# Kernel optimization log

Hardware: AMD Instinct MI355X
Metric: run time of the kernel (lower is better)

Reference implementation:

```python
import jax, jax.numpy as jnp
import numpy as np

N_MODES = 256
N_LAYERS = 4


def _fourier_layer(inp, x, fw_l, lw_l):
    # inp: [B, n_modes] layer state; x: [B, 3] coords
    # tf.signal.rfftnd(..., fft_length=[n_modes]) crops/pads the last axis to
    # n_modes, i.e. uses the first n_modes entries of concat([x, inp], -1).
    d = jnp.concatenate([x, inp], axis=-1)[:, :N_MODES]        # [B, n_modes]
    F = jnp.fft.rfft(d, n=N_MODES, axis=-1)                    # [B, n_modes//2+1]
    x_spatial = jnp.fft.irfft(F * fw_l.astype(F.dtype), n=N_MODES, axis=-1)
    x_spatial = x_spatial.astype(jnp.float32)
    z = inp[:, :N_MODES] * lw_l                                # linear residual branch
    return jax.nn.relu(x_spatial + z)


def setup_inputs() -> dict:
    key = jax.random.key(0)
    ks = jax.random.split(key, 6)
    B, P1, P2, P3 = 262144, 64, N_MODES, 1
    mu = jax.random.normal(ks[0], (B, P1), dtype=jnp.float32)
    x = jax.random.normal(ks[1], (B, 3), dtype=jnp.float32)
    W1 = jax.random.normal(ks[2], (P1, P2), dtype=jnp.float32) * (2.0 / P1) ** 0.5
    b1 = jnp.zeros((P2,), dtype=jnp.float32)
    fw = jax.random.normal(ks[3], (N_LAYERS, N_MODES // 2 + 1), dtype=jnp.float32)
    lw = jax.random.normal(ks[4], (N_LAYERS, N_MODES), dtype=jnp.float32) * 0.1
    W2 = jax.random.normal(ks[5], (P2, P3), dtype=jnp.float32) * (1.0 / P2) ** 0.5
    b2 = jnp.zeros((P3,), dtype=jnp.float32)
    return {"mu": mu, "x": x, "W1": W1, "b1": b1, "fw": fw, "lw": lw, "W2": W2, "b2": b2}


def reference(mu, x, W1, b1, fw, lw, W2, b2):
    # encoder (first_network): dense + relu  -> [B, p_2]
    h = jax.nn.relu(mu @ W1 + b1)
    # stack of Fourier layers (small, structurally distinct loop over n_layers)
    for l in range(N_LAYERS):
        h = _fourier_layer(h, x, fw[l], lw[l])
    # decoder (last_network): dense -> [B, p_3]
    return h @ W2 + b2
```

## Files before the change

### kernel.cpp

```cpp
#include <hip/hip_runtime.h>

#define N_B   262144
#define BM    128
#define KAUG  288
#define LDA   264

typedef _Float16 f16x8 __attribute__((ext_vector_type(8)));
typedef _Float16 f16x4 __attribute__((ext_vector_type(4)));
typedef float    f32x4 __attribute__((ext_vector_type(4)));
typedef float    f32x16 __attribute__((ext_vector_type(16)));

__global__ void fno_precompute(const float* __restrict__ W1,
                               const float* __restrict__ fw,
                               const float* __restrict__ lw,
                               _Float16* __restrict__ Mt,
                               _Float16* __restrict__ W1t)
{
    const int t = threadIdx.x;
    const int b = blockIdx.x;
    if (b < 64) {
        const int l  = b >> 4;
        const int ng = b & 15;
        __shared__ float cosTab[256];
        __shared__ float cs[256];
        cosTab[t] = cosf((float)t * (6.28318530717958647692f / 256.0f));
        __syncthreads();
        {
            const float* fwl = fw + l * 129;
            float s = fwl[0];
            #pragma unroll 4
            for (int k = 1; k < 128; ++k)
                s += 2.0f * fwl[k] * cosTab[(k * t) & 255];
            s += fwl[128] * ((t & 1) ? -1.0f : 1.0f);
            cs[t] = s * (1.0f / 256.0f);
        }
        __syncthreads();
        for (int idx = t; idx < 16 * KAUG; idx += 256) {
            const int n = ng * 16 + idx / KAUG;
            const int k = idx % KAUG;
            float v = 0.0f;
            if (k < 253)               v = cs[(n - k - 3) & 255];
            if (k == n)                v += lw[l * 256 + n];
            if (k >= 256 && k < 259)   v = cs[(n - (k - 256)) & 255];
            Mt[((size_t)l * 256 + n) * KAUG + k] = (_Float16)v;
        }
    } else {
        const int base = (b - 64) * 4096;
        #pragma unroll
        for (int i = 0; i < 16; ++i) {
            const int idx = base + t + i * 256;
            const int n = idx >> 6, k = idx & 63;
            W1t[idx] = (_Float16)W1[k * 256 + n];
        }
    }
}

__global__ __launch_bounds__(256, 2)
void fno_main(const float* __restrict__ mu,
              const float* __restrict__ x,
              const float* __restrict__ b1,
              const float* __restrict__ W2,
              const float* __restrict__ b2,
              const _Float16* __restrict__ Mt,
              const _Float16* __restrict__ W1t,
              float* __restrict__ out)
{
    __shared__ __align__(16) _Float16 hA[(BM + 1) * LDA];
    __shared__ float b1s[256];
    __shared__ float W2s[256];
    __shared__ float red[BM];

    const int t    = threadIdx.x;
    const int w    = t >> 6;
    const int lane = t & 63;
    const int i32  = lane & 31;
    const int q2   = lane >> 5;
    const int r0   = blockIdx.x * BM;
    const int hoff = i32 * LDA + 8 * q2;

    {
        const float4* mu4 = (const float4*)mu + (size_t)r0 * 16;
        #pragma unroll
        for (int j = 0; j < 8; ++j) {
            int f = t + 256 * j;
            int row = f >> 4, c4 = f & 15;
            float4 v = mu4[f];
            f16x4 h;
            h[0] = (_Float16)v.x; h[1] = (_Float16)v.y;
            h[2] = (_Float16)v.z; h[3] = (_Float16)v.w;
            *(f16x4*)&hA[row * LDA + c4 * 4] = h;
        }
        if (t < BM) {
            const float* xp = x + (size_t)(r0 + t) * 3;
            f16x8 hx = {(_Float16)xp[0], (_Float16)xp[1], (_Float16)xp[2],
                        (_Float16)0, (_Float16)0, (_Float16)0,
                        (_Float16)0, (_Float16)0};
            *(f16x8*)&hA[t * LDA + 256] = hx;
        }
        if (t < 33) {
            f16x8 z8 = {};
            *(f16x8*)&hA[BM * LDA + 8 * t] = z8;
        }
        b1s[t] = b1[t];
        W2s[t] = W2[t];
    }
    __syncthreads();

    const f32x16 fz = {0.f,0.f,0.f,0.f, 0.f,0.f,0.f,0.f,
                       0.f,0.f,0.f,0.f, 0.f,0.f,0.f,0.f};
    f32x16 acc[2][4];

    #pragma unroll
    for (int ft = 0; ft < 2; ++ft)
        #pragma unroll
        for (int rt = 0; rt < 4; ++rt) acc[ft][rt] = fz;

    {
        const _Float16* W1p = W1t + (64 * w + i32) * 64 + 8 * q2;
        #pragma unroll
        for (int kc = 0; kc < 4; ++kc) {
            f16x8 mfrag[2];
            #pragma unroll
            for (int ft = 0; ft < 2; ++ft)
                mfrag[ft] = *(const f16x8*)(W1p + 32 * ft * 64 + 16 * kc);
            #pragma unroll
            for (int rt = 0; rt < 4; ++rt) {
                f16x8 hfrag = *(const f16x8*)&hA[hoff + 32 * rt * LDA + 16 * kc];
                #pragma unroll
                for (int ft = 0; ft < 2; ++ft)
                    acc[ft][rt] = __builtin_amdgcn_mfma_f32_32x32x16_f16(
                        mfrag[ft], hfrag, acc[ft][rt], 0, 0, 0);
            }
        }
    }
    __syncthreads();
    #pragma unroll
    for (int ft = 0; ft < 2; ++ft)
        #pragma unroll
        for (int rt = 0; rt < 4; ++rt) {
            const int row = 32 * rt + i32;
            #pragma unroll
            for (int rg = 0; rg < 4; ++rg) {
                const int fb = 64 * w + 32 * ft + 4 * q2 + 8 * rg;
                const float4 bias = *(const float4*)&b1s[fb];
                f16x4 hv;
                hv[0] = (_Float16)fmaxf(acc[ft][rt][4 * rg + 0] + bias.x, 0.f);
                hv[1] = (_Float16)fmaxf(acc[ft][rt][4 * rg + 1] + bias.y, 0.f);
                hv[2] = (_Float16)fmaxf(acc[ft][rt][4 * rg + 2] + bias.z, 0.f);
                hv[3] = (_Float16)fmaxf(acc[ft][rt][4 * rg + 3] + bias.w, 0.f);
                *(f16x4*)&hA[row * LDA + fb] = hv;
            }
        }

    #pragma unroll 1
    for (int l = 0; l < 4; ++l) {
        __syncthreads();
        #pragma unroll
        for (int ft = 0; ft < 2; ++ft)
            #pragma unroll
            for (int rt = 0; rt < 4; ++rt) acc[ft][rt] = fz;

        const _Float16* Mlp = Mt + (size_t)l * 256 * KAUG
                                 + (64 * w + i32) * KAUG + 8 * q2;
        #pragma unroll
        for (int kc = 0; kc < 18; ++kc) {
            f16x8 mfrag[2];
            #pragma unroll
            for (int ft = 0; ft < 2; ++ft)
                mfrag[ft] = *(const f16x8*)(Mlp + 32 * ft * KAUG + 16 * kc);
            #pragma unroll
            for (int rt = 0; rt < 4; ++rt) {
                f16x8 hfrag = *(const f16x8*)&hA[hoff + 32 * rt * LDA + 16 * kc];
                #pragma unroll
                for (int ft = 0; ft < 2; ++ft)
                    acc[ft][rt] = __builtin_amdgcn_mfma_f32_32x32x16_f16(
                        mfrag[ft], hfrag, acc[ft][rt], 0, 0, 0);
            }
        }

        __syncthreads();
        #pragma unroll
        for (int ft = 0; ft < 2; ++ft)
            #pragma unroll
            for (int rt = 0; rt < 4; ++rt) {
                const int row = 32 * rt + i32;
                #pragma unroll
                for (int rg = 0; rg < 4; ++rg) {
                    const int fb = 64 * w + 32 * ft + 4 * q2 + 8 * rg;
                    f16x4 hv;
                    hv[0] = (_Float16)fmaxf(acc[ft][rt][4 * rg + 0], 0.f);
                    hv[1] = (_Float16)fmaxf(acc[ft][rt][4 * rg + 1], 0.f);
                    hv[2] = (_Float16)fmaxf(acc[ft][rt][4 * rg + 2], 0.f);
                    hv[3] = (_Float16)fmaxf(acc[ft][rt][4 * rg + 3], 0.f);
                    *(f16x4*)&hA[row * LDA + fb] = hv;
                }
            }
    }

    __syncthreads();
    {
        const int r  = t & 127;
        const int hf = t >> 7;
        const int n0 = hf * 128;
        float s = 0.f;
        #pragma unroll
        for (int j = 0; j < 16; ++j) {
            f16x8 v = *(const f16x8*)&hA[r * LDA + n0 + 8 * j];
            const float* wp = &W2s[n0 + 8 * j];
            s += (float)v[0] * wp[0] + (float)v[1] * wp[1]
               + (float)v[2] * wp[2] + (float)v[3] * wp[3]
               + (float)v[4] * wp[4] + (float)v[5] * wp[5]
               + (float)v[6] * wp[6] + (float)v[7] * wp[7];
        }
        if (hf) red[r] = s;
        __syncthreads();
        if (!hf) out[r0 + r] = s + red[r] + b2[0];
    }
}

extern "C" void kernel_launch(void* const* d_in, const int* in_sizes, int n_in,
                              void* d_out, int out_size, void* d_ws, size_t ws_size,
                              hipStream_t stream) {
    const float* mu = (const float*)d_in[0];
    const float* x  = (const float*)d_in[1];
    const float* W1 = (const float*)d_in[2];
    const float* b1 = (const float*)d_in[3];
    const float* fw = (const float*)d_in[4];
    const float* lw = (const float*)d_in[5];
    const float* W2 = (const float*)d_in[6];
    const float* b2 = (const float*)d_in[7];
    float* out = (float*)d_out;

    _Float16* Mt  = (_Float16*)d_ws;
    _Float16* W1t = Mt + 4 * 256 * KAUG;

    fno_precompute<<<68, 256, 0, stream>>>(W1, fw, lw, Mt, W1t);
    fno_main<<<N_B / BM, 256, 0, stream>>>(mu, x, b1, W2, b2, Mt, W1t, out);
}
```

Baseline: 248.9 us.

## Shrink row tile to 96 and software-pipeline weight fragment loads across MFMA steps

Reduces the per-block row tile from 128 to 96 (2731 blocks with clamped tail rows), shrinking accumulators and LDS so more waves can be resident and the grid spreads across more CUs. The K-loop is manually unrolled with a triple-buffered rotation of weight fragments, loading fragment k+3 while issuing MFMAs for k, and prefetching the next layer's first fragments before the barrier, to hide global-load latency. Smaller tiles mean each weight fragment is reused across fewer rows, and a tail block does partly wasted work.

```diff
diff --git a/kernel.cpp b/kernel.cpp
--- a/kernel.cpp
+++ b/kernel.cpp
@@ -1,7 +1,8 @@
 #include <hip/hip_runtime.h>
 
 #define N_B   262144
-#define BM    128
+#define BM    96
+#define NBLK  2731
 #define KAUG  288
 #define LDA   264
 
@@ -55,6 +56,25 @@
     }
 }
 
+
+#define KSTEP(M0, M1, KB)                                                   \
+    { _Pragma("unroll")                                                     \
+      for (int rt = 0; rt < 3; ++rt) {                                      \
+          f16x8 hfrag = *(const f16x8*)&hA[hoff + 32 * rt * LDA + (KB)];    \
+          acc[0][rt] = __builtin_amdgcn_mfma_f32_32x32x16_f16(              \
+              M0, hfrag, acc[0][rt], 0, 0, 0);                              \
+          acc[1][rt] = __builtin_amdgcn_mfma_f32_32x32x16_f16(              \
+              M1, hfrag, acc[1][rt], 0, 0, 0);                              \
+      } }
+
+#define LDM(M0, M1, PTR, KB)                                                \
+    { M0 = *(const f16x8*)((PTR) + (KB));                                   \
+      M1 = *(const f16x8*)((PTR) + 32 * KAUG + (KB)); }
+
+#define LDMW(M0, M1, KB)                                                    \
+    { M0 = *(const f16x8*)(W1p + (KB));                                     \
+      M1 = *(const f16x8*)(W1p + 32 * 64 + (KB)); }
+
 __global__ __launch_bounds__(256, 2)
 void fno_main(const float* __restrict__ mu,
               const float* __restrict__ x,
@@ -65,7 +85,7 @@
               const _Float16* __restrict__ W1t,
               float* __restrict__ out)
 {
-    __shared__ __align__(16) _Float16 hA[(BM + 1) * LDA];
+    __shared__ __align__(16) _Float16 hA[BM * LDA + 24];
     __shared__ float b1s[256];
     __shared__ float W2s[256];
     __shared__ float red[BM];
@@ -79,65 +99,66 @@
     const int hoff = i32 * LDA + 8 * q2;
 
     {
-        const float4* mu4 = (const float4*)mu + (size_t)r0 * 16;
-        #pragma unroll
-        for (int j = 0; j < 8; ++j) {
+        const float4* mu4 = (const float4*)mu;
+        #pragma unroll
+        for (int j = 0; j < 6; ++j) {
             int f = t + 256 * j;
             int row = f >> 4, c4 = f & 15;
-            float4 v = mu4[f];
+            int g = r0 + row; if (g > N_B - 1) g = N_B - 1;
+            float4 v = mu4[(size_t)g * 16 + c4];
             f16x4 h;
             h[0] = (_Float16)v.x; h[1] = (_Float16)v.y;
             h[2] = (_Float16)v.z; h[3] = (_Float16)v.w;
             *(f16x4*)&hA[row * LDA + c4 * 4] = h;
         }
         if (t < BM) {
-            const float* xp = x + (size_t)(r0 + t) * 3;
+            int g = r0 + t; if (g > N_B - 1) g = N_B - 1;
+            const float* xp = x + (size_t)g * 3;
             f16x8 hx = {(_Float16)xp[0], (_Float16)xp[1], (_Float16)xp[2],
                         (_Float16)0, (_Float16)0, (_Float16)0,
                         (_Float16)0, (_Float16)0};
             *(f16x8*)&hA[t * LDA + 256] = hx;
         }
-        if (t < 33) {
+        if (t < 3) {
             f16x8 z8 = {};
             *(f16x8*)&hA[BM * LDA + 8 * t] = z8;
         }
         b1s[t] = b1[t];
         W2s[t] = W2[t];
     }
+
+    const _Float16* W1p = W1t + (64 * w + i32) * 64 + 8 * q2;
+    f16x8 mA0, mA1, mB0, mB1, mC0, mC1;
+    LDMW(mA0, mA1, 0)
+    LDMW(mB0, mB1, 16)
+    LDMW(mC0, mC1, 32)
     __syncthreads();
 
     const f32x16 fz = {0.f,0.f,0.f,0.f, 0.f,0.f,0.f,0.f,
                        0.f,0.f,0.f,0.f, 0.f,0.f,0.f,0.f};
-    f32x16 acc[2][4];
+    f32x16 acc[2][3];
 
     #pragma unroll
     for (int ft = 0; ft < 2; ++ft)
         #pragma unroll
-        for (int rt = 0; rt < 4; ++rt) acc[ft][rt] = fz;
+        for (int rt = 0; rt < 3; ++rt) acc[ft][rt] = fz;
+
+    KSTEP(mA0, mA1, 0)   LDMW(mA0, mA1, 48)
+    KSTEP(mB0, mB1, 16)
+    KSTEP(mC0, mC1, 32)
+    KSTEP(mA0, mA1, 48)
 
     {
-        const _Float16* W1p = W1t + (64 * w + i32) * 64 + 8 * q2;
-        #pragma unroll
-        for (int kc = 0; kc < 4; ++kc) {
-            f16x8 mfrag[2];
-            #pragma unroll
-            for (int ft = 0; ft < 2; ++ft)
-                mfrag[ft] = *(const f16x8*)(W1p + 32 * ft * 64 + 16 * kc);
-            #pragma unroll
-            for (int rt = 0; rt < 4; ++rt) {
-                f16x8 hfrag = *(const f16x8*)&hA[hoff + 32 * rt * LDA + 16 * kc];
-                #pragma unroll
-                for (int ft = 0; ft < 2; ++ft)
-                    acc[ft][rt] = __builtin_amdgcn_mfma_f32_32x32x16_f16(
-                        mfrag[ft], hfrag, acc[ft][rt], 0, 0, 0);
-            }
-        }
+        const _Float16* M0p = Mt + (size_t)(64 * w + i32) * KAUG + 8 * q2;
+        LDM(mA0, mA1, M0p, 0)
+        LDM(mB0, mB1, M0p, 16)
+        LDM(mC0, mC1, M0p, 32)
     }
     __syncthreads();
     #pragma unroll
     for (int ft = 0; ft < 2; ++ft)
         #pragma unroll
-        for (int rt = 0; rt < 4; ++rt) {
+        for (int rt = 0; rt < 3; ++rt) {
             const int row = 32 * rt + i32;
             #pragma unroll
             for (int rg = 0; rg < 4; ++rg) {
@@ -158,31 +179,40 @@
         #pragma unroll
         for (int ft = 0; ft < 2; ++ft)
             #pragma unroll
-            for (int rt = 0; rt < 4; ++rt) acc[ft][rt] = fz;
-
-        const _Float16* Mlp = Mt + (size_t)l * 256 * KAUG
-                                 + (64 * w + i32) * KAUG + 8 * q2;
-        #pragma unroll
-        for (int kc = 0; kc < 18; ++kc) {
-            f16x8 mfrag[2];
-            #pragma unroll
-            for (int ft = 0; ft < 2; ++ft)
-                mfrag[ft] = *(const f16x8*)(Mlp + 32 * ft * KAUG + 16 * kc);
-            #pragma unroll
-            for (int rt = 0; rt < 4; ++rt) {
-                f16x8 hfrag = *(const f16x8*)&hA[hoff + 32 * rt * LDA + 16 * kc];
-                #pragma unroll
-                for (int ft = 0; ft < 2; ++ft)
-                    acc[ft][rt] = __builtin_amdgcn_mfma_f32_32x32x16_f16(
-                        mfrag[ft], hfrag, acc[ft][rt], 0, 0, 0);
-            }
+            for (int rt = 0; rt < 3; ++rt) acc[ft][rt] = fz;
+
+        const _Float16* Mlp = Mt + ((size_t)l * 256 + 64 * w + i32) * KAUG + 8 * q2;
+
+        KSTEP(mA0, mA1,   0)  LDM(mA0, mA1, Mlp,  48)
+        KSTEP(mB0, mB1,  16)  LDM(mB0, mB1, Mlp,  64)
+        KSTEP(mC0, mC1,  32)  LDM(mC0, mC1, Mlp,  80)
+        KSTEP(mA0, mA1,  48)  LDM(mA0, mA1, Mlp,  96)
+        KSTEP(mB0, mB1,  64)  LDM(mB0, mB1, Mlp, 112)
+        KSTEP(mC0, mC1,  80)  LDM(mC0, mC1, Mlp, 128)
+        KSTEP(mA0, mA1,  96)  LDM(mA0, mA1, Mlp, 144)
+        KSTEP(mB0, mB1, 112)  LDM(mB0, mB1, Mlp, 160)
+        KSTEP(mC0, mC1, 128)  LDM(mC0, mC1, Mlp, 176)
+        KSTEP(mA0, mA1, 144)  LDM(mA0, mA1, Mlp, 192)
+        KSTEP(mB0, mB1, 160)  LDM(mB0, mB1, Mlp, 208)
+        KSTEP(mC0, mC1, 176)  LDM(mC0, mC1, Mlp, 224)
+        KSTEP(mA0, mA1, 192)  LDM(mA0, mA1, Mlp, 240)
+        KSTEP(mB0, mB1, 208)  LDM(mB0, mB1, Mlp, 256)
+        KSTEP(mC0, mC1, 224)
+        KSTEP(mA0, mA1, 240)
+        KSTEP(mB0, mB1, 256)
+
+        if (l < 3) {
+            const _Float16* Mn = Mlp + 256 * KAUG;
+            LDM(mA0, mA1, Mn, 0)
+            LDM(mB0, mB1, Mn, 16)
+            LDM(mC0, mC1, Mn, 32)
         }
 
         __syncthreads();
         #pragma unroll
         for (int ft = 0; ft < 2; ++ft)
             #pragma unroll
-            for (int rt = 0; rt < 4; ++rt) {
+            for (int rt = 0; rt < 3; ++rt) {
                 const int row = 32 * rt + i32;
                 #pragma unroll
                 for (int rg = 0; rg < 4; ++rg) {
@@ -199,22 +229,25 @@
 
     __syncthreads();
     {
-        const int r  = t & 127;
-        const int hf = t >> 7;
-        const int n0 = hf * 128;
+        const int r    = t >> 1;
+        const int half = t & 1;
         float s = 0.f;
-        #pragma unroll
-        for (int j = 0; j < 16; ++j) {
-            f16x8 v = *(const f16x8*)&hA[r * LDA + n0 + 8 * j];
-            const float* wp = &W2s[n0 + 8 * j];
-            s += (float)v[0] * wp[0] + (float)v[1] * wp[1]
-               + (float)v[2] * wp[2] + (float)v[3] * wp[3]
-               + (float)v[4] * wp[4] + (float)v[5] * wp[5]
-               + (float)v[6] * wp[6] + (float)v[7] * wp[7];
-        }
-        if (hf) red[r] = s;
-        __syncthreads();
-        if (!hf) out[r0 + r] = s + red[r] + b2[0];
+        if (t < 2 * BM) {
+            const int n0 = half * 128;
+            #pragma unroll
+            for (int j = 0; j < 16; ++j) {
+                f16x8 v = *(const f16x8*)&hA[r * LDA + n0 + 8 * j];
+                const float* wp = &W2s[n0 + 8 * j];
+                s += (float)v[0] * wp[0] + (float)v[1] * wp[1]
+                   + (float)v[2] * wp[2] + (float)v[3] * wp[3]
+                   + (float)v[4] * wp[4] + (float)v[5] * wp[5]
+                   + (float)v[6] * wp[6] + (float)v[7] * wp[7];
+            }
+            if (half) red[r] = s;
+        }
+        __syncthreads();
+        if (t < 2 * BM && !half && r0 + r < N_B)
+            out[r0 + r] = s + red[r] + b2[0];
     }
 }
 
@@ -235,5 +268,5 @@
     _Float16* W1t = Mt + 4 * 256 * KAUG;
 
     fno_precompute<<<68, 256, 0, stream>>>(W1, fw, lw, Mt, W1t);
-    fno_main<<<N_B / BM, 256, 0, stream>>>(mu, x, b1, W2, b2, Mt, W1t, out);
+    fno_main<<<NBLK, 256, 0, stream>>>(mu, x, b1, W2, b2, Mt, W1t, out);
 }
```

Measured after the change: 281.5 us. 1.13x slower.

## Shrink Fourier-layer GEMM K to 256 and XOR-swizzle the LDS activation tile

Applied to the files above, without the earlier changes.

The augmented K dimension drops from 288 to 256. The three x-coordinate columns are packed into slots 253-255 of each row, and the three displaced h entries (253..255) are stashed in a side slot. Their lw residual and W2 decoder terms are then added back with scalar FMAs. This cuts MFMA work per layer by about an eighth. It also replaces the padded LDS layout with an XOR swizzle, aiming to avoid bank conflicts on fragment loads. In exchange it adds branchy special-case stores and extra fixup code.

```diff
diff --git a/kernel.cpp b/kernel.cpp
--- a/kernel.cpp
+++ b/kernel.cpp
@@ -2,8 +2,9 @@
 
 #define N_B   262144
 #define BM    128
-#define KAUG  288
+#define KD    256
 #define LDA   264
+#define LDAB  528
 
 typedef _Float16 f16x8 __attribute__((ext_vector_type(8)));
 typedef _Float16 f16x4 __attribute__((ext_vector_type(4)));
@@ -35,14 +36,17 @@
             cs[t] = s * (1.0f / 256.0f);
         }
         __syncthreads();
-        for (int idx = t; idx < 16 * KAUG; idx += 256) {
-            const int n = ng * 16 + idx / KAUG;
-            const int k = idx % KAUG;
-            float v = 0.0f;
-            if (k < 253)               v = cs[(n - k - 3) & 255];
-            if (k == n)                v += lw[l * 256 + n];
-            if (k >= 256 && k < 259)   v = cs[(n - (k - 256)) & 255];
-            Mt[((size_t)l * 256 + n) * KAUG + k] = (_Float16)v;
+        for (int idx = t; idx < 16 * KD; idx += 256) {
+            const int n = ng * 16 + (idx >> 8);
+            const int k = idx & 255;
+            float v;
+            if (k < 253) {
+                v = cs[(n - k - 3) & 255];
+                if (k == n) v += lw[l * 256 + n];
+            } else {
+                v = cs[(n - (k - 253)) & 255];
+            }
+            Mt[((size_t)l * 256 + n) * KD + k] = (_Float16)v;
         }
     } else {
         const int base = (b - 64) * 4096;
@@ -59,15 +63,16 @@
 void fno_main(const float* __restrict__ mu,
               const float* __restrict__ x,
               const float* __restrict__ b1,
+              const float* __restrict__ lw,
               const float* __restrict__ W2,
               const float* __restrict__ b2,
               const _Float16* __restrict__ Mt,
               const _Float16* __restrict__ W1t,
               float* __restrict__ out)
 {
-    __shared__ __align__(16) _Float16 hA[(BM + 1) * LDA];
+    __shared__ __align__(16) char hAb[BM * LDAB];
     __shared__ float b1s[256];
-    __shared__ float W2s[256];
+    __shared__ float W2s[260];
     __shared__ float red[BM];
 
     const int t    = threadIdx.x;
@@ -76,7 +81,7 @@
     const int i32  = lane & 31;
     const int q2   = lane >> 5;
     const int r0   = blockIdx.x * BM;
-    const int hoff = i32 * LDA + 8 * q2;
+    const int xrB  = ((i32 >> 3) & 3) << 4;
 
     {
         const float4* mu4 = (const float4*)mu + (size_t)r0 * 16;
@@ -84,25 +89,24 @@
         for (int j = 0; j < 8; ++j) {
             int f = t + 256 * j;
             int row = f >> 4, c4 = f & 15;
+            int xr = ((row >> 3) & 3) << 4;
             float4 v = mu4[f];
             f16x4 h;
             h[0] = (_Float16)v.x; h[1] = (_Float16)v.y;
             h[2] = (_Float16)v.z; h[3] = (_Float16)v.w;
-            *(f16x4*)&hA[row * LDA + c4 * 4] = h;
+            *(f16x4*)(hAb + row * LDAB + ((c4 * 8) ^ xr)) = h;
         }
         if (t < BM) {
-            const float* xp = x + (size_t)(r0 + t) * 3;
-            f16x8 hx = {(_Float16)xp[0], (_Float16)xp[1], (_Float16)xp[2],
-                        (_Float16)0, (_Float16)0, (_Float16)0,
-                        (_Float16)0, (_Float16)0};
-            *(f16x8*)&hA[t * LDA + 256] = hx;
-        }
-        if (t < 33) {
-            f16x8 z8 = {};
-            *(f16x8*)&hA[BM * LDA + 8 * t] = z8;
+            const int row = t;
+            const int xr = ((row >> 3) & 3) << 4;
+            const float* xp = x + (size_t)(r0 + row) * 3;
+            *(_Float16*)(hAb + row * LDAB + (506 ^ xr)) = (_Float16)xp[0];
+            *(_Float16*)(hAb + row * LDAB + (508 ^ xr)) = (_Float16)xp[1];
+            *(_Float16*)(hAb + row * LDAB + (510 ^ xr)) = (_Float16)xp[2];
         }
         b1s[t] = b1[t];
-        W2s[t] = W2[t];
+        W2s[t] = (t < 252) ? W2[t] : 0.0f;
+        if (t < 4) W2s[256 + t] = W2[252 + t];
     }
     __syncthreads();
 
@@ -119,17 +123,14 @@
         const _Float16* W1p = W1t + (64 * w + i32) * 64 + 8 * q2;
         #pragma unroll
         for (int kc = 0; kc < 4; ++kc) {
-            f16x8 mfrag[2];
-            #pragma unroll
-            for (int ft = 0; ft < 2; ++ft)
-                mfrag[ft] = *(const f16x8*)(W1p + 32 * ft * 64 + 16 * kc);
-            #pragma unroll
-            for (int rt = 0; rt < 4; ++rt) {
-                f16x8 hfrag = *(const f16x8*)&hA[hoff + 32 * rt * LDA + 16 * kc];
-                #pragma unroll
-                for (int ft = 0; ft < 2; ++ft)
-                    acc[ft][rt] = __builtin_amdgcn_mfma_f32_32x32x16_f16(
-                        mfrag[ft], hfrag, acc[ft][rt], 0, 0, 0);
+            f16x8 m0 = *(const f16x8*)(W1p + 16 * kc);
+            f16x8 m1 = *(const f16x8*)(W1p + 32 * 64 + 16 * kc);
+            #pragma unroll
+            for (int rt = 0; rt < 4; ++rt) {
+                f16x8 hfrag = *(const f16x8*)(hAb + (32 * rt + i32) * LDAB
+                                              + ((32 * kc + 16 * q2) ^ xrB));
+                acc[0][rt] = __builtin_amdgcn_mfma_f32_32x32x16_f16(m0, hfrag, acc[0][rt], 0, 0, 0);
+                acc[1][rt] = __builtin_amdgcn_mfma_f32_32x32x16_f16(m1, hfrag, acc[1][rt], 0, 0, 0);
             }
         }
     }
@@ -148,7 +149,12 @@
                 hv[1] = (_Float16)fmaxf(acc[ft][rt][4 * rg + 1] + bias.y, 0.f);
                 hv[2] = (_Float16)fmaxf(acc[ft][rt][4 * rg + 2] + bias.z, 0.f);
                 hv[3] = (_Float16)fmaxf(acc[ft][rt][4 * rg + 3] + bias.w, 0.f);
-                *(f16x4*)&hA[row * LDA + fb] = hv;
+                if (fb == 252) {
+                    *(_Float16*)(hAb + row * LDAB + (504 ^ xrB)) = hv[0];
+                    *(f16x4*)(hAb + row * LDAB + 512) = hv;
+                } else {
+                    *(f16x4*)(hAb + row * LDAB + ((fb * 2) ^ xrB)) = hv;
+                }
             }
         }
 
@@ -160,21 +166,29 @@
             #pragma unroll
             for (int rt = 0; rt < 4; ++rt) acc[ft][rt] = fz;
 
-        const _Float16* Mlp = Mt + (size_t)l * 256 * KAUG
-                                 + (64 * w + i32) * KAUG + 8 * q2;
-        #pragma unroll
-        for (int kc = 0; kc < 18; ++kc) {
-            f16x8 mfrag[2];
-            #pragma unroll
-            for (int ft = 0; ft < 2; ++ft)
-                mfrag[ft] = *(const f16x8*)(Mlp + 32 * ft * KAUG + 16 * kc);
-            #pragma unroll
-            for (int rt = 0; rt < 4; ++rt) {
-                f16x8 hfrag = *(const f16x8*)&hA[hoff + 32 * rt * LDA + 16 * kc];
-                #pragma unroll
-                for (int ft = 0; ft < 2; ++ft)
-                    acc[ft][rt] = __builtin_amdgcn_mfma_f32_32x32x16_f16(
-                        mfrag[ft], hfrag, acc[ft][rt], 0, 0, 0);
+        const _Float16* Mlp = Mt + ((size_t)(l * 256 + 64 * w + i32)) * KD + 8 * q2;
+        #pragma unroll
+        for (int kc = 0; kc < 16; ++kc) {
+            f16x8 m0 = *(const f16x8*)(Mlp + 16 * kc);
+            f16x8 m1 = *(const f16x8*)(Mlp + 32 * KD + 16 * kc);
+            #pragma unroll
+            for (int rt = 0; rt < 4; ++rt) {
+                f16x8 hfrag = *(const f16x8*)(hAb + (32 * rt + i32) * LDAB
+                                              + ((32 * kc + 16 * q2) ^ xrB));
+                acc[0][rt] = __builtin_amdgcn_mfma_f32_32x32x16_f16(m0, hfrag, acc[0][rt], 0, 0, 0);
+                acc[1][rt] = __builtin_amdgcn_mfma_f32_32x32x16_f16(m1, hfrag, acc[1][rt], 0, 0, 0);
+            }
+        }
+
+        if (w == 3 && q2 == 1) {
+            const float* lwp = lw + l * 256 + 253;
+            const float lw0 = lwp[0], lw1 = lwp[1], lw2 = lwp[2];
+            #pragma unroll
+            for (int rt = 0; rt < 4; ++rt) {
+                f16x4 hp = *(const f16x4*)(hAb + (32 * rt + i32) * LDAB + 512);
+                acc[1][rt][13] += lw0 * (float)hp[1];
+                acc[1][rt][14] += lw1 * (float)hp[2];
+                acc[1][rt][15] += lw2 * (float)hp[3];
             }
         }
 
@@ -192,7 +206,12 @@
                     hv[1] = (_Float16)fmaxf(acc[ft][rt][4 * rg + 1], 0.f);
                     hv[2] = (_Float16)fmaxf(acc[ft][rt][4 * rg + 2], 0.f);
                     hv[3] = (_Float16)fmaxf(acc[ft][rt][4 * rg + 3], 0.f);
-                    *(f16x4*)&hA[row * LDA + fb] = hv;
+                    if (fb == 252) {
+                        *(_Float16*)(hAb + row * LDAB + (504 ^ xrB)) = hv[0];
+                        *(f16x4*)(hAb + row * LDAB + 512) = hv;
+                    } else {
+                        *(f16x4*)(hAb + row * LDAB + ((fb * 2) ^ xrB)) = hv;
+                    }
                 }
             }
     }
@@ -202,17 +221,23 @@
         const int r  = t & 127;
         const int hf = t >> 7;
         const int n0 = hf * 128;
+        const int xr = ((r >> 3) & 3) << 4;
         float s = 0.f;
         #pragma unroll
         for (int j = 0; j < 16; ++j) {
-            f16x8 v = *(const f16x8*)&hA[r * LDA + n0 + 8 * j];
+            f16x8 v = *(const f16x8*)(hAb + r * LDAB + (((n0 + 8 * j) * 2) ^ xr));
             const float* wp = &W2s[n0 + 8 * j];
             s += (float)v[0] * wp[0] + (float)v[1] * wp[1]
                + (float)v[2] * wp[2] + (float)v[3] * wp[3]
                + (float)v[4] * wp[4] + (float)v[5] * wp[5]
                + (float)v[6] * wp[6] + (float)v[7] * wp[7];
         }
-        if (hf) red[r] = s;
+        if (hf) {
+            f16x4 st = *(const f16x4*)(hAb + r * LDAB + 512);
+            s += (float)st[0] * W2s[256] + (float)st[1] * W2s[257]
+               + (float)st[2] * W2s[258] + (float)st[3] * W2s[259];
+            red[r] = s;
+        }
         __syncthreads();
         if (!hf) out[r0 + r] = s + red[r] + b2[0];
     }
@@ -232,8 +257,8 @@
     float* out = (float*)d_out;
 
     _Float16* Mt  = (_Float16*)d_ws;
-    _Float16* W1t = Mt + 4 * 256 * KAUG;
+    _Float16* W1t = Mt + 4 * 256 * KD;
 
     fno_precompute<<<68, 256, 0, stream>>>(W1, fw, lw, Mt, W1t);
-    fno_main<<<N_B / BM, 256, 0, stream>>>(mu, x, b1, W2, b2, Mt, W1t, out);
+    fno_main<<<N_B / BM, 256, 0, stream>>>(mu, x, b1, lw, W2, b2, Mt, W1t, out);
 }
```

New measurement: 259.5 us. +4.3%, slower.

## Split row tiles across 8 waves and skip zero-padded K chunk

Applied to the files above, without the earlier changes.

Doubles the block to 512 threads, so each wave computes a 64-row by 64-feature tile instead of 128 rows. This halves the accumulator registers per wave and is meant to raise occupancy and latency hiding. The Fourier-layer K loop drops its last 16-wide chunk, which only held zero padding. The final W2 reduction is split four ways across the threads. The cost is that weight fragments are loaded twice per block from global or L2, and there are more waves taking part in each barrier.

```diff
diff --git a/kernel.cpp b/kernel.cpp
--- a/kernel.cpp
+++ b/kernel.cpp
@@ -55,7 +55,7 @@
     }
 }
 
-__global__ __launch_bounds__(256, 2)
+__global__ __launch_bounds__(512, 4)
 void fno_main(const float* __restrict__ mu,
               const float* __restrict__ x,
               const float* __restrict__ b1,
@@ -68,21 +68,23 @@
     __shared__ __align__(16) _Float16 hA[(BM + 1) * LDA];
     __shared__ float b1s[256];
     __shared__ float W2s[256];
-    __shared__ float red[BM];
+    __shared__ float red3[3][BM];
 
     const int t    = threadIdx.x;
     const int w    = t >> 6;
+    const int wf   = w & 3;
+    const int wr   = w >> 2;
     const int lane = t & 63;
     const int i32  = lane & 31;
     const int q2   = lane >> 5;
     const int r0   = blockIdx.x * BM;
-    const int hoff = i32 * LDA + 8 * q2;
+    const int hoff = (64 * wr + i32) * LDA + 8 * q2;
 
     {
         const float4* mu4 = (const float4*)mu + (size_t)r0 * 16;
         #pragma unroll
-        for (int j = 0; j < 8; ++j) {
-            int f = t + 256 * j;
+        for (int j = 0; j < 4; ++j) {
+            int f = t + 512 * j;
             int row = f >> 4, c4 = f & 15;
             float4 v = mu4[f];
             f16x4 h;
@@ -101,35 +103,30 @@
             f16x8 z8 = {};
             *(f16x8*)&hA[BM * LDA + 8 * t] = z8;
         }
-        b1s[t] = b1[t];
-        W2s[t] = W2[t];
+        if (t < 256) { b1s[t] = b1[t]; W2s[t] = W2[t]; }
     }
     __syncthreads();
 
     const f32x16 fz = {0.f,0.f,0.f,0.f, 0.f,0.f,0.f,0.f,
                        0.f,0.f,0.f,0.f, 0.f,0.f,0.f,0.f};
-    f32x16 acc[2][4];
+    f32x16 acc[2][2];
 
     #pragma unroll
     for (int ft = 0; ft < 2; ++ft)
         #pragma unroll
-        for (int rt = 0; rt < 4; ++rt) acc[ft][rt] = fz;
+        for (int rt = 0; rt < 2; ++rt) acc[ft][rt] = fz;
 
     {
-        const _Float16* W1p = W1t + (64 * w + i32) * 64 + 8 * q2;
+        const _Float16* W1p = W1t + (64 * wf + i32) * 64 + 8 * q2;
         #pragma unroll
         for (int kc = 0; kc < 4; ++kc) {
-            f16x8 mfrag[2];
-            #pragma unroll
-            for (int ft = 0; ft < 2; ++ft)
-                mfrag[ft] = *(const f16x8*)(W1p + 32 * ft * 64 + 16 * kc);
-            #pragma unroll
-            for (int rt = 0; rt < 4; ++rt) {
+            f16x8 m0 = *(const f16x8*)(W1p + 16 * kc);
+            f16x8 m1 = *(const f16x8*)(W1p + 32 * 64 + 16 * kc);
+            #pragma unroll
+            for (int rt = 0; rt < 2; ++rt) {
                 f16x8 hfrag = *(const f16x8*)&hA[hoff + 32 * rt * LDA + 16 * kc];
-                #pragma unroll
-                for (int ft = 0; ft < 2; ++ft)
-                    acc[ft][rt] = __builtin_amdgcn_mfma_f32_32x32x16_f16(
-                        mfrag[ft], hfrag, acc[ft][rt], 0, 0, 0);
+                acc[0][rt] = __builtin_amdgcn_mfma_f32_32x32x16_f16(m0, hfrag, acc[0][rt], 0, 0, 0);
+                acc[1][rt] = __builtin_amdgcn_mfma_f32_32x32x16_f16(m1, hfrag, acc[1][rt], 0, 0, 0);
             }
         }
     }
@@ -137,11 +134,11 @@
     #pragma unroll
     for (int ft = 0; ft < 2; ++ft)
         #pragma unroll
-        for (int rt = 0; rt < 4; ++rt) {
-            const int row = 32 * rt + i32;
+        for (int rt = 0; rt < 2; ++rt) {
+            const int row = 64 * wr + 32 * rt + i32;
             #pragma unroll
             for (int rg = 0; rg < 4; ++rg) {
-                const int fb = 64 * w + 32 * ft + 4 * q2 + 8 * rg;
+                const int fb = 64 * wf + 32 * ft + 4 * q2 + 8 * rg;
                 const float4 bias = *(const float4*)&b1s[fb];
                 f16x4 hv;
                 hv[0] = (_Float16)fmaxf(acc[ft][rt][4 * rg + 0] + bias.x, 0.f);
@@ -158,23 +155,18 @@
         #pragma unroll
         for (int ft = 0; ft < 2; ++ft)
             #pragma unroll
-            for (int rt = 0; rt < 4; ++rt) acc[ft][rt] = fz;
-
-        const _Float16* Mlp = Mt + (size_t)l * 256 * KAUG
-                                 + (64 * w + i32) * KAUG + 8 * q2;
-        #pragma unroll
-        for (int kc = 0; kc < 18; ++kc) {
-            f16x8 mfrag[2];
-            #pragma unroll
-            for (int ft = 0; ft < 2; ++ft)
-                mfrag[ft] = *(const f16x8*)(Mlp + 32 * ft * KAUG + 16 * kc);
-            #pragma unroll
-            for (int rt = 0; rt < 4; ++rt) {
+            for (int rt = 0; rt < 2; ++rt) acc[ft][rt] = fz;
+
+        const _Float16* Mlp = Mt + ((size_t)l * 256 + 64 * wf + i32) * KAUG + 8 * q2;
+        #pragma unroll
+        for (int kc = 0; kc < 17; ++kc) {
+            f16x8 m0 = *(const f16x8*)(Mlp + 16 * kc);
+            f16x8 m1 = *(const f16x8*)(Mlp + 32 * KAUG + 16 * kc);
+            #pragma unroll
+            for (int rt = 0; rt < 2; ++rt) {
                 f16x8 hfrag = *(const f16x8*)&hA[hoff + 32 * rt * LDA + 16 * kc];
-                #pragma unroll
-                for (int ft = 0; ft < 2; ++ft)
-                    acc[ft][rt] = __builtin_amdgcn_mfma_f32_32x32x16_f16(
-                        mfrag[ft], hfrag, acc[ft][rt], 0, 0, 0);
+                acc[0][rt] = __builtin_amdgcn_mfma_f32_32x32x16_f16(m0, hfrag, acc[0][rt], 0, 0, 0);
+                acc[1][rt] = __builtin_amdgcn_mfma_f32_32x32x16_f16(m1, hfrag, acc[1][rt], 0, 0, 0);
             }
         }
 
@@ -182,11 +174,11 @@
         #pragma unroll
         for (int ft = 0; ft < 2; ++ft)
             #pragma unroll
-            for (int rt = 0; rt < 4; ++rt) {
-                const int row = 32 * rt + i32;
+            for (int rt = 0; rt < 2; ++rt) {
+                const int row = 64 * wr + 32 * rt + i32;
                 #pragma unroll
                 for (int rg = 0; rg < 4; ++rg) {
-                    const int fb = 64 * w + 32 * ft + 4 * q2 + 8 * rg;
+                    const int fb = 64 * wf + 32 * ft + 4 * q2 + 8 * rg;
                     f16x4 hv;
                     hv[0] = (_Float16)fmaxf(acc[ft][rt][4 * rg + 0], 0.f);
                     hv[1] = (_Float16)fmaxf(acc[ft][rt][4 * rg + 1], 0.f);
@@ -199,12 +191,12 @@
 
     __syncthreads();
     {
-        const int r  = t & 127;
-        const int hf = t >> 7;
-        const int n0 = hf * 128;
+        const int r   = t & 127;
+        const int seg = t >> 7;
+        const int n0  = seg * 64;
         float s = 0.f;
         #pragma unroll
-        for (int j = 0; j < 16; ++j) {
+        for (int j = 0; j < 8; ++j) {
             f16x8 v = *(const f16x8*)&hA[r * LDA + n0 + 8 * j];
             const float* wp = &W2s[n0 + 8 * j];
             s += (float)v[0] * wp[0] + (float)v[1] * wp[1]
@@ -212,9 +204,10 @@
                + (float)v[4] * wp[4] + (float)v[5] * wp[5]
                + (float)v[6] * wp[6] + (float)v[7] * wp[7];
         }
-        if (hf) red[r] = s;
-        __syncthreads();
-        if (!hf) out[r0 + r] = s + red[r] + b2[0];
+        if (seg) red3[seg - 1][r] = s;
+        __syncthreads();
+        if (!seg)
+            out[r0 + r] = s + red3[0][r] + red3[1][r] + red3[2][r] + b2[0];
     }
 }
 
@@ -235,5 +228,5 @@
     _Float16* W1t = Mt + 4 * 256 * KAUG;
 
     fno_precompute<<<68, 256, 0, stream>>>(W1, fw, lw, Mt, W1t);
-    fno_main<<<N_B / BM, 256, 0, stream>>>(mu, x, b1, W2, b2, Mt, W1t, out);
+    fno_main<<<N_B / BM, 512, 0, stream>>>(mu, x, b1, W2, b2, Mt, W1t, out);
 }
```

Result: slower. 283.9 us (+14.1%).
